# Optimization experiments

Hardware: AMD Instinct MI355X
Metric: run time of the kernel (lower is better)

The kernel has to match this reference:

```python
import jax, jax.numpy as jnp
import numpy as np

B, C, H, W = 16, 512, 64, 64
HEADS = 8
DIL = 2  # dilation of the 3x3 depthwise conv (padding == dilation -> shape preserving)


def setup_inputs() -> dict:
    key = jax.random.key(0)
    ks = jax.random.split(key, 4)
    x = jax.random.normal(ks[0], (B, C, H, W), jnp.float32)
    # kaiming-normal-ish scales (fan_out, relu)
    w_qkv = jax.random.normal(ks[1], (3 * C, C), jnp.float32) * (2.0 / C) ** 0.5  # 1x1 conv weight
    w_dw = jax.random.normal(ks[2], (C, 3, 3), jnp.float32) * (2.0 / 9.0) ** 0.5  # depthwise 3x3
    w_out = jax.random.normal(ks[3], (C, C), jnp.float32) * (2.0 / C) ** 0.5      # 1x1 conv weight
    temperature = jnp.sqrt(jnp.asarray(C // HEADS, jnp.float32))                  # init sqrt(dim_per_head)
    return {"x": x, "w_qkv": w_qkv, "w_dw": w_dw, "w_out": w_out, "temperature": temperature}


def _dw_conv(y, w_dw):
    # depthwise dilated 3x3 conv, padding=dilation -> same spatial size
    rhs = w_dw[:, None, :, :]  # [C,1,3,3]
    return jax.lax.conv_general_dilated(
        y, rhs, window_strides=(1, 1), padding=((DIL, DIL), (DIL, DIL)),
        rhs_dilation=(DIL, DIL), feature_group_count=y.shape[1],
        dimension_numbers=("NCHW", "OIHW", "NCHW"))


def reference(x, w_qkv, w_dw, w_out, temperature):
    b, c, h, w = x.shape
    n = h * w
    d = c // HEADS
    # 1x1 qkv projection (bias-free conv == einsum)
    qkv = jnp.einsum("oc,bchw->bohw", w_qkv, x)  # [B,3C,H,W]
    q, k, v = jnp.split(qkv, 3, axis=1)
    # same depthwise conv applied to q,k,v: fold into batch, conv once
    qkv3 = _dw_conv(jnp.concatenate([q, k, v], axis=0), w_dw)  # [3B,C,H,W]
    q, k, v = jnp.split(qkv3, 3, axis=0)
    q = q.reshape(b, HEADS, d, n)
    k = k.reshape(b, HEADS, d, n)
    v = v.reshape(b, HEADS, d, n)
    # L2 normalize along the per-head channel dim (dim=2), eps=1e-12 like F.normalize
    l2 = lambda t: t / jnp.maximum(jnp.linalg.norm(t, axis=2, keepdims=True), 1e-12)
    q = l2(q)
    k = l2(k)
    # cross-covariance attention: [B,heads,d,d]
    attn = jnp.einsum("bhdn,bhen->bhde", q, k) / jnp.maximum(temperature, 1e-5)
    attn = jax.nn.softmax(attn, axis=-1)
    # dropout is identity in eval mode
    out = jnp.einsum("bhde,bhen->bhdn", attn, v).reshape(b, c, h, w)
    return jnp.einsum("oc,bchw->bohw", w_out, out)
```

## Files before the change

### kernel.cpp

```cpp
#include <hip/hip_runtime.h>

typedef __attribute__((ext_vector_type(8))) short bf16x8;
typedef __attribute__((ext_vector_type(8))) unsigned short ushort8;
typedef __attribute__((ext_vector_type(4))) float f32x4;
typedef __attribute__((ext_vector_type(4))) unsigned int u32x4;
typedef __attribute__((ext_vector_type(2))) unsigned int u32x2;

__device__ __forceinline__ float bf2f(unsigned short u) {
  union { unsigned int i; float f; } v; v.i = ((unsigned int)u) << 16; return v.f;
}
__device__ __forceinline__ float asf(unsigned int u) {
  union { unsigned int i; float f; } v; v.i = u; return v.f;
}
__device__ __forceinline__ unsigned short f2bf(float f) {
  union { float f; unsigned int i; } v; v.f = f;
  unsigned int u = v.i;
  return (unsigned short)((u + 0x7FFFu + ((u >> 16) & 1u)) >> 16);
}
__device__ __forceinline__ void gload16(const void* g, void* l) {
  __builtin_amdgcn_global_load_lds(
      (const __attribute__((address_space(1))) void*)g,
      (__attribute__((address_space(3))) void*)l, 16, 0, 0);
}

__global__ __launch_bounds__(256) void cvt_f32_bf16(const float* __restrict__ s,
                                                    unsigned short* __restrict__ d, int n) {
  int i = blockIdx.x * 256 + threadIdx.x;
  if (i < n) d[i] = f2bf(s[i]);
}

__global__ __launch_bounds__(256) void transpose_x(const float* __restrict__ x,
                                                   unsigned short* __restrict__ xt) {
  __shared__ float tile[64][65];
  const int b = blockIdx.z, ct = blockIdx.y, nt = blockIdx.x;
  const int t = threadIdx.x;
  const int r0 = t >> 6, col = t & 63;
  const float* src = x + ((size_t)b * 512 + ct * 64) * 4096 + nt * 64;
#pragma unroll
  for (int i = 0; i < 16; ++i) {
    int r = i * 4 + r0;
    tile[r][col] = src[(size_t)r * 4096 + col];
  }
  __syncthreads();
  unsigned short* dst = xt + ((size_t)b * 4096 + nt * 64) * 512 + ct * 64;
#pragma unroll
  for (int i = 0; i < 16; ++i) {
    int n = i * 4 + r0;
    dst[(size_t)n * 512 + col] = f2bf(tile[col][n]);
  }
}

__global__ __launch_bounds__(512, 1) void gemm_qkv_8ph(const unsigned short* __restrict__ A,
                                                       const unsigned short* __restrict__ B,
                                                       unsigned short* __restrict__ C) {
  __shared__ unsigned short lA[2][256 * 64];
  __shared__ unsigned short lB[2][256 * 64];
  const int gx = gridDim.x;
  const int nwg = gx * gridDim.y;
  int flat = blockIdx.x + gx * blockIdx.y;
  flat = (flat & 7) * (nwg >> 3) + (flat >> 3);
  const int bx = flat % gx;
  const int by = flat / gx;
  const size_t m0 = (size_t)by * 256;
  const size_t n0 = (size_t)bx * 256;

  const int t = threadIdx.x;
  const int lane = t & 63;
  const int wid = t >> 6;
  const int wm = wid >> 2, wn = wid & 3;
  const int ro = lane & 15, kq = lane >> 4;

  const int srow = t >> 3;
  const int sslot = t & 7;
  const int kslot = sslot ^ (srow & 7);

  auto stageA = [&](int kt, int h, int bbuf) {
    char* d = (char*)(&lA[bbuf][0]) + ((h * 128 + srow) * 64 + sslot * 8) * 2;
    const unsigned short* g = A + (m0 + h * 128 + srow) * 512 + kt * 64 + kslot * 8;
    gload16(g, d);
    gload16(g + (size_t)64 * 512, d + 64 * 128);
  };
  auto stageB = [&](int kt, int h, int bbuf) {
    char* d = (char*)(&lB[bbuf][0]) + ((h * 128 + srow) * 64 + sslot * 8) * 2;
    const unsigned short* g = B + (n0 + h * 128 + srow) * 512 + kt * 64 + kslot * 8;
    gload16(g, d);
    gload16(g + (size_t)64 * 512, d + 64 * 128);
  };

  f32x4 acc[8][4] = {};

  stageA(0, 0, 0); stageA(0, 1, 0);
  stageB(0, 0, 0); stageB(0, 1, 0);
  stageA(1, 0, 1); stageA(1, 1, 1);
  asm volatile("s_waitcnt vmcnt(4)" ::: "memory");
  __builtin_amdgcn_s_barrier();

#pragma unroll 1
  for (int kt = 0; kt < 8; ++kt) {
    const int c = kt & 1;
    const unsigned short* pa = &lA[c][0];
    const unsigned short* pb = &lB[c][0];
    const int slot0 = kq ^ (ro & 7);
    const int slot1 = (4 + kq) ^ (ro & 7);

    bf16x8 a0[8], a1[8], b0, b1, b2, b3;
#pragma unroll
    for (int i = 0; i < 8; ++i)
      a0[i] = *(const bf16x8*)&pa[(wm * 128 + i * 16 + ro) * 64 + slot0 * 8];
    b0 = *(const bf16x8*)&pb[(wn * 64 + 0 * 16 + ro) * 64 + slot0 * 8];
    b1 = *(const bf16x8*)&pb[(wn * 64 + 1 * 16 + ro) * 64 + slot0 * 8];
    if (kt + 1 < 8) stageB(kt + 1, 0, c ^ 1);
    asm volatile("" ::: "memory");
    __builtin_amdgcn_s_barrier();
    asm volatile("s_waitcnt lgkmcnt(0)" ::: "memory");
    __builtin_amdgcn_s_setprio(1);
#pragma unroll
    for (int i = 0; i < 8; ++i) {
      acc[i][0] = __builtin_amdgcn_mfma_f32_16x16x32_bf16(a0[i], b0, acc[i][0], 0, 0, 0);
      acc[i][1] = __builtin_amdgcn_mfma_f32_16x16x32_bf16(a0[i], b1, acc[i][1], 0, 0, 0);
    }
    __builtin_amdgcn_s_setprio(0);

    b2 = *(const bf16x8*)&pb[(wn * 64 + 2 * 16 + ro) * 64 + slot0 * 8];
    b3 = *(const bf16x8*)&pb[(wn * 64 + 3 * 16 + ro) * 64 + slot0 * 8];
    if (kt + 1 < 8) stageB(kt + 1, 1, c ^ 1);
    asm volatile("" ::: "memory");
    __builtin_amdgcn_s_barrier();
    asm volatile("s_waitcnt lgkmcnt(0)" ::: "memory");
    __builtin_amdgcn_s_setprio(1);
#pragma unroll
    for (int i = 0; i < 8; ++i) {
      acc[i][2] = __builtin_amdgcn_mfma_f32_16x16x32_bf16(a0[i], b2, acc[i][2], 0, 0, 0);
      acc[i][3] = __builtin_amdgcn_mfma_f32_16x16x32_bf16(a0[i], b3, acc[i][3], 0, 0, 0);
    }
    __builtin_amdgcn_s_setprio(0);

#pragma unroll
    for (int i = 0; i < 8; ++i)
      a1[i] = *(const bf16x8*)&pa[(wm * 128 + i * 16 + ro) * 64 + slot1 * 8];
    b0 = *(const bf16x8*)&pb[(wn * 64 + 0 * 16 + ro) * 64 + slot1 * 8];
    b1 = *(const bf16x8*)&pb[(wn * 64 + 1 * 16 + ro) * 64 + slot1 * 8];
    asm volatile("s_waitcnt lgkmcnt(0)" ::: "memory");
    __builtin_amdgcn_s_barrier();
    __builtin_amdgcn_s_setprio(1);
#pragma unroll
    for (int i = 0; i < 8; ++i) {
      acc[i][0] = __builtin_amdgcn_mfma_f32_16x16x32_bf16(a1[i], b0, acc[i][0], 0, 0, 0);
      acc[i][1] = __builtin_amdgcn_mfma_f32_16x16x32_bf16(a1[i], b1, acc[i][1], 0, 0, 0);
    }
    __builtin_amdgcn_s_setprio(0);

    b2 = *(const bf16x8*)&pb[(wn * 64 + 2 * 16 + ro) * 64 + slot1 * 8];
    b3 = *(const bf16x8*)&pb[(wn * 64 + 3 * 16 + ro) * 64 + slot1 * 8];
    if (kt + 2 < 8) { stageA(kt + 2, 0, c); stageA(kt + 2, 1, c); }
    asm volatile("s_waitcnt lgkmcnt(0)" ::: "memory");
    if (kt < 6)       asm volatile("s_waitcnt vmcnt(4)" ::: "memory");
    else if (kt == 6) asm volatile("s_waitcnt vmcnt(0)" ::: "memory");
    __builtin_amdgcn_s_barrier();
    __builtin_amdgcn_s_setprio(1);
#pragma unroll
    for (int i = 0; i < 8; ++i) {
      acc[i][2] = __builtin_amdgcn_mfma_f32_16x16x32_bf16(a1[i], b2, acc[i][2], 0, 0, 0);
      acc[i][3] = __builtin_amdgcn_mfma_f32_16x16x32_bf16(a1[i], b3, acc[i][3], 0, 0, 0);
    }
    __builtin_amdgcn_s_setprio(0);
  }

#pragma unroll
  for (int i = 0; i < 8; ++i)
#pragma unroll
    for (int j = 0; j < 4; ++j)
#pragma unroll
      for (int r = 0; r < 4; ++r) {
        size_t row = m0 + wm * 128 + i * 16 + (kq << 2) + r;
        size_t col = n0 + wn * 64 + j * 16 + ro;
        C[row * 1536 + col] = f2bf(acc[i][j][r]);
      }
}

template <bool BF16OUT>
__global__ __launch_bounds__(256) void gemm_bt(const unsigned short* __restrict__ A,
                                               const unsigned short* __restrict__ B,
                                               void* __restrict__ Cv, int K, int ldc,
                                               size_t sA, size_t sB, size_t sC) {
  __shared__ unsigned short lA[2][128 * 32];
  __shared__ unsigned short lB[2][128 * 32];
  const int gx = gridDim.x, gy = gridDim.y;
  const int nwg = gx * gy * gridDim.z;
  int flat = blockIdx.x + gx * (blockIdx.y + gy * blockIdx.z);
  flat = (flat & 7) * (nwg >> 3) + (flat >> 3);
  const int bx = flat % gx;
  const int rem = flat / gx;
  const int by = rem % gy;
  const int bz = rem / gy;

  const int t = threadIdx.x;
  const int lane = t & 63;
  const int wv = t >> 6, wr = wv >> 1, wc = wv & 1;
  const size_t m0 = (size_t)by * 128;
  const size_t n0 = (size_t)bx * 128;
  A += (size_t)bz * sA;
  B += (size_t)bz * sB;
  const unsigned short* ga = A + (m0 + (t >> 2)) * (size_t)K + (t & 3) * 8;
  const unsigned short* gb = B + (n0 + (t >> 2)) * (size_t)K + (t & 3) * 8;
  const size_t gstep = (size_t)64 * K;

  f32x4 acc[4][4] = {};

  auto stage = [&](int kt, int bbuf) {
    const unsigned short* pa = ga + kt * 32;
    const unsigned short* pb = gb + kt * 32;
    char* da = (char*)(&lA[bbuf][0]) + t * 16;
    char* db = (char*)(&lB[bbuf][0]) + t * 16;
    gload16(pa, da);
    gload16(pa + gstep, da + 4096);
    gload16(pb, db);
    gload16(pb + gstep, db + 4096);
  };

  const int nk = K >> 5;
  stage(0, 0);
  __syncthreads();
  int buf = 0;
  for (int kt = 0; kt < nk; ++kt) {
    if (kt + 1 < nk) stage(kt + 1, buf ^ 1);
    const unsigned short* pa = &lA[buf][0];
    const unsigned short* pb = &lB[buf][0];
    const int ro = lane & 15, ko = (lane >> 4) * 8;
    bf16x8 af[4], bv[4];
#pragma unroll
    for (int i = 0; i < 4; ++i) af[i] = *(const bf16x8*)&pa[(wr * 64 + i * 16 + ro) * 32 + ko];
#pragma unroll
    for (int i = 0; i < 4; ++i) bv[i] = *(const bf16x8*)&pb[(wc * 64 + i * 16 + ro) * 32 + ko];
#pragma unroll
    for (int i = 0; i < 4; ++i)
#pragma unroll
      for (int j = 0; j < 4; ++j)
        acc[i][j] = __builtin_amdgcn_mfma_f32_16x16x32_bf16(af[i], bv[j], acc[i][j], 0, 0, 0);
    __syncthreads();
    buf ^= 1;
  }

  if constexpr (BF16OUT) {
    unsigned short* C = (unsigned short*)Cv + (size_t)bz * sC;
#pragma unroll
    for (int i = 0; i < 4; ++i)
#pragma unroll
      for (int j = 0; j < 4; ++j)
#pragma unroll
        for (int r = 0; r < 4; ++r) {
          size_t row = m0 + wr * 64 + i * 16 + ((lane >> 4) << 2) + r;
          size_t col = n0 + wc * 64 + j * 16 + (lane & 15);
          C[row * (size_t)ldc + col] = f2bf(acc[i][j][r]);
        }
  } else {
    float* C = (float*)Cv + (size_t)bz * sC;
#pragma unroll
    for (int i = 0; i < 4; ++i)
#pragma unroll
      for (int j = 0; j < 4; ++j)
#pragma unroll
        for (int r = 0; r < 4; ++r) {
          size_t row = m0 + wr * 64 + i * 16 + ((lane >> 4) << 2) + r;
          size_t col = n0 + wc * 64 + j * 16 + (lane & 15);
          C[row * (size_t)ldc + col] = acc[i][j][r];
        }
  }
}

struct Row3h { u32x2 v[3]; };

__global__ __launch_bounds__(256) void dwconv_norm(const unsigned short* __restrict__ Y,
                                                   const float* __restrict__ wdw,
                                                   unsigned short* __restrict__ Qb,
                                                   unsigned short* __restrict__ Kb,
                                                   unsigned short* __restrict__ Vb) {
  const int t = threadIdx.x, lane = t & 63, wv = t >> 6;
  const int bid = blockIdx.x;
  const int lbid = (bid & 7) * 384 + (bid >> 3);
  const int wid = lbid * 4 + wv;
  const int sub = wid & 3;
  const int x = (wid >> 2) & 63;
  const int grp = wid >> 8;
  const int par = sub >> 1, chhalf = sub & 1;
  const int b = grp / 3, part = grp - b * 3;
  const int c0 = chhalf * 256 + (lane >> 4) * 64 + (lane & 15) * 4;

  float wr[36];
  const float* wp = wdw + c0 * 9;
#pragma unroll
  for (int i = 0; i < 9; ++i) {
    f32x4 q = *(const f32x4*)(wp + i * 4);
    wr[i * 4 + 0] = q[0]; wr[i * 4 + 1] = q[1];
    wr[i * 4 + 2] = q[2]; wr[i * 4 + 3] = q[3];
  }

  const size_t ybase = (size_t)b * 4096 * 1536 + part * 512 + c0;
  const bool okm = (x >= 2), okp = (x <= 61);
  const int xm = okm ? x - 2 : x;
  const int xp = okp ? x + 2 : x;

  auto loadrow = [&](int yy) -> Row3h {
    Row3h r;
    const bool oky = ((unsigned)yy < 64u);
    const int yyc = oky ? yy : 0;
    const size_t rb = ybase + (size_t)(yyc * 64) * 1536;
    u32x2 a = *(const u32x2*)(Y + rb + (size_t)xm * 1536);
    u32x2 c = *(const u32x2*)(Y + rb + (size_t)x * 1536);
    u32x2 d = *(const u32x2*)(Y + rb + (size_t)xp * 1536);
    r.v[0] = a & ((oky && okm) ? 0xFFFFFFFFu : 0u);
    r.v[1] = c & (oky ? 0xFFFFFFFFu : 0u);
    r.v[2] = d & ((oky && okp) ? 0xFFFFFFFFu : 0u);
    return r;
  };

  Row3h W[3];
#pragma unroll
  for (int xt = 0; xt < 3; ++xt) W[0].v[xt] = (u32x2)(0u);
  W[1] = loadrow(par);
  W[2] = loadrow(par + 2);

  unsigned short* dst0 = (part == 0 ? Qb : (part == 1 ? Kb : Vb)) +
                         ((size_t)b * 4096 + x) * 512 + c0;

#pragma unroll
  for (int i = 0; i < 32; ++i) {
    const int y = par + 2 * i;
    float acc[4] = {0.f, 0.f, 0.f, 0.f};
#pragma unroll
    for (int r = 0; r < 3; ++r) {
      const Row3h& R = W[(i + r) % 3];
#pragma unroll
      for (int xt = 0; xt < 3; ++xt) {
        const int tap = r * 3 + xt;
        const u32x2 v = R.v[xt];
#pragma unroll
        for (int m = 0; m < 2; ++m) {
          const unsigned int w2 = v[m];
          acc[2 * m]     += asf(w2 << 16)         * wr[(2 * m) * 9 + tap];
          acc[2 * m + 1] += asf(w2 & 0xFFFF0000u) * wr[(2 * m + 1) * 9 + tap];
        }
      }
    }
    if (part < 2) {
      float ss = 0.f;
#pragma unroll
      for (int j = 0; j < 4; ++j) ss += acc[j] * acc[j];
      ss += __shfl_xor(ss, 1);
      ss += __shfl_xor(ss, 2);
      ss += __shfl_xor(ss, 4);
      ss += __shfl_xor(ss, 8);
      const float rcp = 1.f / fmaxf(sqrtf(ss), 1e-12f);
#pragma unroll
      for (int j = 0; j < 4; ++j) acc[j] *= rcp;
    }
    u32x2 pk;
    pk[0] = (unsigned int)f2bf(acc[0]) | ((unsigned int)f2bf(acc[1]) << 16);
    pk[1] = (unsigned int)f2bf(acc[2]) | ((unsigned int)f2bf(acc[3]) << 16);
    *(u32x2*)(dst0 + (size_t)y * 64 * 512) = pk;
    if (i < 31) W[i % 3] = loadrow(y + 4);
  }
}

__global__ __launch_bounds__(256) void attn_partial(const unsigned short* __restrict__ Qb,
                                                    const unsigned short* __restrict__ Kb,
                                                    float* __restrict__ Spart) {
  __shared__ unsigned short sQ[4][64][72];
  __shared__ unsigned short sK[4][64][72];
  const int t = threadIdx.x, lane = t & 63, wv = t >> 6;
  const int bh = blockIdx.x >> 2;
  const int s = (blockIdx.x & 3) * 4 + wv;
  const int b = bh >> 3, h = bh & 7;
  const unsigned short* qbase = Qb + ((size_t)b * 4096) * 512 + h * 64;
  const unsigned short* kbase = Kb + ((size_t)b * 4096) * 512 + h * 64;
  f32x4 acc[4][4] = {};
  for (int ch = 0; ch < 4; ++ch) {
    const int n0 = s * 256 + ch * 64;
    const unsigned short* qp = qbase + (size_t)(n0 + lane) * 512;
    const unsigned short* kp = kbase + (size_t)(n0 + lane) * 512;
    ushort8 qv[8], kv[8];
#pragma unroll
    for (int v = 0; v < 8; ++v) qv[v] = *(const ushort8*)(qp + v * 8);
#pragma unroll
    for (int v = 0; v < 8; ++v) kv[v] = *(const ushort8*)(kp + v * 8);
#pragma unroll
    for (int v = 0; v < 8; ++v)
#pragma unroll
      for (int j = 0; j < 8; ++j) {
        sQ[wv][v * 8 + j][lane] = qv[v][j];
        sK[wv][v * 8 + j][lane] = kv[v][j];
      }
    __syncthreads();
    const int ro = lane & 15, ko = (lane >> 4) * 8;
#pragma unroll
    for (int ks = 0; ks < 2; ++ks) {
      bf16x8 af[4], bv[4];
#pragma unroll
      for (int i = 0; i < 4; ++i) af[i] = *(const bf16x8*)&sQ[wv][i * 16 + ro][ks * 32 + ko];
#pragma unroll
      for (int i = 0; i < 4; ++i) bv[i] = *(const bf16x8*)&sK[wv][i * 16 + ro][ks * 32 + ko];
#pragma unroll
      for (int i = 0; i < 4; ++i)
#pragma unroll
        for (int j = 0; j < 4; ++j)
          acc[i][j] = __builtin_amdgcn_mfma_f32_16x16x32_bf16(af[i], bv[j], acc[i][j], 0, 0, 0);
    }
    __syncthreads();
  }
  float* dst = Spart + ((size_t)bh * 16 + s) * 4096;
#pragma unroll
  for (int i = 0; i < 4; ++i)
#pragma unroll
    for (int j = 0; j < 4; ++j)
#pragma unroll
      for (int r = 0; r < 4; ++r) {
        int d = i * 16 + ((lane >> 4) << 2) + r;
        int e = j * 16 + (lane & 15);
        dst[d * 64 + e] = acc[i][j][r];
      }
}

__global__ __launch_bounds__(256) void softmax_attn(const float* __restrict__ Spart,
                                                    const float* __restrict__ tptr,
                                                    unsigned short* __restrict__ attn) {
  const int bh = blockIdx.x, t = threadIdx.x;
  const int d = t >> 2, eb = (t & 3) << 4;
  const float inv_t = 1.f / fmaxf(tptr[0], 1e-5f);
  float v[16];
#pragma unroll
  for (int i = 0; i < 16; ++i) v[i] = 0.f;
  for (int s = 0; s < 16; ++s) {
    const f32x4* p = (const f32x4*)(Spart + ((size_t)bh * 16 + s) * 4096 + d * 64 + eb);
#pragma unroll
    for (int i = 0; i < 4; ++i) {
      f32x4 q = p[i];
      v[i * 4 + 0] += q[0]; v[i * 4 + 1] += q[1];
      v[i * 4 + 2] += q[2]; v[i * 4 + 3] += q[3];
    }
  }
  float mx = -1e30f;
#pragma unroll
  for (int i = 0; i < 16; ++i) { v[i] *= inv_t; mx = fmaxf(mx, v[i]); }
  mx = fmaxf(mx, __shfl_xor(mx, 1));
  mx = fmaxf(mx, __shfl_xor(mx, 2));
  float sm = 0.f;
#pragma unroll
  for (int i = 0; i < 16; ++i) { v[i] = __expf(v[i] - mx); sm += v[i]; }
  sm += __shfl_xor(sm, 1);
  sm += __shfl_xor(sm, 2);
  const float r = 1.f / sm;
  ushort8 pk0, pk1;
#pragma unroll
  for (int i = 0; i < 8; ++i) { pk0[i] = f2bf(v[i] * r); pk1[i] = f2bf(v[8 + i] * r); }
  ushort8* dst = (ushort8*)(attn + (size_t)bh * 4096 + d * 64 + eb);
  dst[0] = pk0; dst[1] = pk1;
}

__global__ __launch_bounds__(256) void make_w2(const unsigned short* __restrict__ attn,
                                               const float* __restrict__ w_out,
                                               unsigned short* __restrict__ w2) {
  __shared__ float sA[4096];
  const int bx = blockIdx.x;
  const int bh = bx >> 1, half = bx & 1;
  const int b = bh >> 3, h = bh & 7;
  const int t = threadIdx.x;
  for (int i = t; i < 4096; i += 256) sA[i] = bf2f(attn[(size_t)bh * 4096 + i]);
  __syncthreads();
  const int o = half * 256 + t;
  float w[64];
  const float* wp = w_out + (size_t)o * 512 + h * 64;
#pragma unroll
  for (int i = 0; i < 64; i += 4) {
    f32x4 q = *(const f32x4*)(wp + i);
    w[i] = q[0]; w[i + 1] = q[1]; w[i + 2] = q[2]; w[i + 3] = q[3];
  }
  unsigned short* dst = w2 + ((size_t)b * 512 + o) * 512 + h * 64;
#pragma unroll 1
  for (int eg = 0; eg < 8; ++eg) {
    ushort8 pk;
#pragma unroll
    for (int ee = 0; ee < 8; ++ee) {
      const int e = eg * 8 + ee;
      float acc = 0.f;
#pragma unroll
      for (int dd = 0; dd < 64; ++dd) acc += w[dd] * sA[dd * 64 + e];
      pk[ee] = f2bf(acc);
    }
    *(ushort8*)(dst + eg * 8) = pk;
  }
}

extern "C" void kernel_launch(void* const* d_in, const int* in_sizes, int n_in,
                              void* d_out, int out_size, void* d_ws, size_t ws_size,
                              hipStream_t stream) {
  const float* x     = (const float*)d_in[0];
  const float* w_qkv = (const float*)d_in[1];
  const float* w_dw  = (const float*)d_in[2];
  const float* w_out = (const float*)d_in[3];
  const float* temp  = (const float*)d_in[4];
  float* out = (float*)d_out;

  char* ws = (char*)d_ws;
  const size_t MB = 1024 * 1024;
  unsigned short* Xt    = (unsigned short*)(ws);
  float*          Spart = (float*)(ws);
  unsigned short* attn  = (unsigned short*)(ws + 32 * MB);
  unsigned short* w2    = (unsigned short*)(ws + 33 * MB);
  unsigned short* Y     = (unsigned short*)(ws + 64 * MB);
  unsigned short* Qb    = (unsigned short*)(ws + 256 * MB);
  unsigned short* Kb    = (unsigned short*)(ws + 320 * MB);
  unsigned short* Vb    = (unsigned short*)(ws + 384 * MB);
  unsigned short* Wq    = (unsigned short*)(ws + 448 * MB);

  cvt_f32_bf16<<<3072, 256, 0, stream>>>(w_qkv, Wq, 1536 * 512);
  transpose_x<<<dim3(64, 8, 16), 256, 0, stream>>>(x, Xt);
  gemm_qkv_8ph<<<dim3(6, 256), 512, 0, stream>>>(Xt, Wq, Y);
  dwconv_norm<<<3072, 256, 0, stream>>>(Y, w_dw, Qb, Kb, Vb);
  attn_partial<<<512, 256, 0, stream>>>(Qb, Kb, Spart);
  softmax_attn<<<128, 256, 0, stream>>>(Spart, temp, attn);
  make_w2<<<256, 256, 0, stream>>>(attn, w_out, w2);
  gemm_bt<false><<<dim3(32, 4, 16), 256, 0, stream>>>(
      w2, Vb, out, 512, 4096,
      (size_t)512 * 512, (size_t)4096 * 512, (size_t)512 * 4096);
}
```

Measured before the change: 423.0 us.

## Fuse x transpose and bf16 conversion into QKV GEMM A-tile loading

Removes the separate transpose_x kernel. The QKV GEMM now reads fp32 x directly from its NCHW layout, converts it to bf16 with packed convert instructions and writes it into swizzled LDS through registers, replacing the async global-to-LDS copies. This saves one full write and re-read of the transposed activation tensor plus a kernel launch, at the cost of extra VGPRs, a register-staged A pipeline and reworked vmcnt waits. The depthwise conv kernel is also changed to use packed f32x2 arithmetic and hardware bf16 pack conversion.

```diff
diff --git a/kernel.cpp b/kernel.cpp
--- a/kernel.cpp
+++ b/kernel.cpp
@@ -3,6 +3,7 @@
 typedef __attribute__((ext_vector_type(8))) short bf16x8;
 typedef __attribute__((ext_vector_type(8))) unsigned short ushort8;
 typedef __attribute__((ext_vector_type(4))) float f32x4;
+typedef __attribute__((ext_vector_type(2))) float f32x2;
 typedef __attribute__((ext_vector_type(4))) unsigned int u32x4;
 typedef __attribute__((ext_vector_type(2))) unsigned int u32x2;
 
@@ -29,28 +30,7 @@
   if (i < n) d[i] = f2bf(s[i]);
 }
 
-__global__ __launch_bounds__(256) void transpose_x(const float* __restrict__ x,
-                                                   unsigned short* __restrict__ xt) {
-  __shared__ float tile[64][65];
-  const int b = blockIdx.z, ct = blockIdx.y, nt = blockIdx.x;
-  const int t = threadIdx.x;
-  const int r0 = t >> 6, col = t & 63;
-  const float* src = x + ((size_t)b * 512 + ct * 64) * 4096 + nt * 64;
-#pragma unroll
-  for (int i = 0; i < 16; ++i) {
-    int r = i * 4 + r0;
-    tile[r][col] = src[(size_t)r * 4096 + col];
-  }
-  __syncthreads();
-  unsigned short* dst = xt + ((size_t)b * 4096 + nt * 64) * 512 + ct * 64;
-#pragma unroll
-  for (int i = 0; i < 16; ++i) {
-    int n = i * 4 + r0;
-    dst[(size_t)n * 512 + col] = f2bf(tile[col][n]);
-  }
-}
-
-__global__ __launch_bounds__(512, 1) void gemm_qkv_8ph(const unsigned short* __restrict__ A,
+__global__ __launch_bounds__(512, 1) void gemm_qkv_8ph(const float* __restrict__ X,
                                                        const unsigned short* __restrict__ B,
                                                        unsigned short* __restrict__ C) {
   __shared__ unsigned short lA[2][256 * 64];
@@ -70,16 +50,11 @@
   const int wm = wid >> 2, wn = wid & 3;
   const int ro = lane & 15, kq = lane >> 4;
 
+  const float* xA = X + ((size_t)(m0 >> 12) << 21) + (m0 & 4095);
+
   const int srow = t >> 3;
   const int sslot = t & 7;
   const int kslot = sslot ^ (srow & 7);
-
-  auto stageA = [&](int kt, int h, int bbuf) {
-    char* d = (char*)(&lA[bbuf][0]) + ((h * 128 + srow) * 64 + sslot * 8) * 2;
-    const unsigned short* g = A + (m0 + h * 128 + srow) * 512 + kt * 64 + kslot * 8;
-    gload16(g, d);
-    gload16(g + (size_t)64 * 512, d + 64 * 128);
-  };
   auto stageB = [&](int kt, int h, int bbuf) {
     char* d = (char*)(&lB[bbuf][0]) + ((h * 128 + srow) * 64 + sslot * 8) * 2;
     const unsigned short* g = B + (n0 + h * 128 + srow) * 512 + kt * 64 + kslot * 8;
@@ -87,12 +62,42 @@
     gload16(g + (size_t)64 * 512, d + 64 * 128);
   };
 
+  float av[16];
+  auto loadAh = [&](int kt2, int h) {
+#pragma unroll
+    for (int g2 = 0; g2 < 2; ++g2) {
+      const float* p = xA + (size_t)(kt2 * 64 + wid * 8) * 4096 + h * 128 + g2 * 64 + lane;
+#pragma unroll
+      for (int j = 0; j < 8; ++j)
+        av[g2 * 8 + j] = p[(size_t)j * 4096];
+    }
+  };
+  auto writeAh = [&](int h, int bbuf) {
+#pragma unroll
+    for (int g2 = 0; g2 < 2; ++g2) {
+      unsigned int p0, p1, p2, p3;
+      asm("v_cvt_pk_bf16_f32 %0, %1, %2" : "=v"(p0) : "v"(av[g2*8+0]), "v"(av[g2*8+1]));
+      asm("v_cvt_pk_bf16_f32 %0, %1, %2" : "=v"(p1) : "v"(av[g2*8+2]), "v"(av[g2*8+3]));
+      asm("v_cvt_pk_bf16_f32 %0, %1, %2" : "=v"(p2) : "v"(av[g2*8+4]), "v"(av[g2*8+5]));
+      asm("v_cvt_pk_bf16_f32 %0, %1, %2" : "=v"(p3) : "v"(av[g2*8+6]), "v"(av[g2*8+7]));
+      const int row = h * 128 + g2 * 64 + lane;
+      char* d = (char*)(&lA[bbuf][0]) + row * 128 + (wid ^ (lane & 7)) * 16;
+      u32x4 w4; w4[0] = p0; w4[1] = p1; w4[2] = p2; w4[3] = p3;
+      *(u32x4*)d = w4;
+    }
+  };
+
   f32x4 acc[8][4] = {};
 
-  stageA(0, 0, 0); stageA(0, 1, 0);
   stageB(0, 0, 0); stageB(0, 1, 0);
-  stageA(1, 0, 1); stageA(1, 1, 1);
-  asm volatile("s_waitcnt vmcnt(4)" ::: "memory");
+  loadAh(0, 0);
+  asm volatile("s_waitcnt vmcnt(0)" ::: "memory");
+  writeAh(0, 0);
+  loadAh(0, 1);
+  asm volatile("s_waitcnt vmcnt(0)" ::: "memory");
+  writeAh(1, 0);
+  loadAh(1, 0);
+  asm volatile("s_waitcnt lgkmcnt(0)" ::: "memory");
   __builtin_amdgcn_s_barrier();
 
 #pragma unroll 1
@@ -103,24 +108,30 @@
     const int slot0 = kq ^ (ro & 7);
     const int slot1 = (4 + kq) ^ (ro & 7);
 
-    bf16x8 a0[8], a1[8], b0, b1, b2, b3;
+    bf16x8 a[8], b0, b1;
 #pragma unroll
     for (int i = 0; i < 8; ++i)
-      a0[i] = *(const bf16x8*)&pa[(wm * 128 + i * 16 + ro) * 64 + slot0 * 8];
+      a[i] = *(const bf16x8*)&pa[(wm * 128 + i * 16 + ro) * 64 + slot0 * 8];
     b0 = *(const bf16x8*)&pb[(wn * 64 + 0 * 16 + ro) * 64 + slot0 * 8];
     b1 = *(const bf16x8*)&pb[(wn * 64 + 1 * 16 + ro) * 64 + slot0 * 8];
     if (kt + 1 < 8) stageB(kt + 1, 0, c ^ 1);
     asm volatile("" ::: "memory");
     __builtin_amdgcn_s_barrier();
+    if (kt + 1 < 8) {
+      asm volatile("s_waitcnt vmcnt(0)" ::: "memory");
+      writeAh(0, c ^ 1);
+      loadAh(kt + 1, 1);
+    }
     asm volatile("s_waitcnt lgkmcnt(0)" ::: "memory");
     __builtin_amdgcn_s_setprio(1);
 #pragma unroll
     for (int i = 0; i < 8; ++i) {
-      acc[i][0] = __builtin_amdgcn_mfma_f32_16x16x32_bf16(a0[i], b0, acc[i][0], 0, 0, 0);
-      acc[i][1] = __builtin_amdgcn_mfma_f32_16x16x32_bf16(a0[i], b1, acc[i][1], 0, 0, 0);
+      acc[i][0] = __builtin_amdgcn_mfma_f32_16x16x32_bf16(a[i], b0, acc[i][0], 0, 0, 0);
+      acc[i][1] = __builtin_amdgcn_mfma_f32_16x16x32_bf16(a[i], b1, acc[i][1], 0, 0, 0);
     }
     __builtin_amdgcn_s_setprio(0);
 
+    bf16x8 b2, b3;
     b2 = *(const bf16x8*)&pb[(wn * 64 + 2 * 16 + ro) * 64 + slot0 * 8];
     b3 = *(const bf16x8*)&pb[(wn * 64 + 3 * 16 + ro) * 64 + slot0 * 8];
     if (kt + 1 < 8) stageB(kt + 1, 1, c ^ 1);
@@ -130,38 +141,42 @@
     __builtin_amdgcn_s_setprio(1);
 #pragma unroll
     for (int i = 0; i < 8; ++i) {
-      acc[i][2] = __builtin_amdgcn_mfma_f32_16x16x32_bf16(a0[i], b2, acc[i][2], 0, 0, 0);
-      acc[i][3] = __builtin_amdgcn_mfma_f32_16x16x32_bf16(a0[i], b3, acc[i][3], 0, 0, 0);
+      acc[i][2] = __builtin_amdgcn_mfma_f32_16x16x32_bf16(a[i], b2, acc[i][2], 0, 0, 0);
+      acc[i][3] = __builtin_amdgcn_mfma_f32_16x16x32_bf16(a[i], b3, acc[i][3], 0, 0, 0);
     }
     __builtin_amdgcn_s_setprio(0);
 
 #pragma unroll
     for (int i = 0; i < 8; ++i)
-      a1[i] = *(const bf16x8*)&pa[(wm * 128 + i * 16 + ro) * 64 + slot1 * 8];
+      a[i] = *(const bf16x8*)&pa[(wm * 128 + i * 16 + ro) * 64 + slot1 * 8];
     b0 = *(const bf16x8*)&pb[(wn * 64 + 0 * 16 + ro) * 64 + slot1 * 8];
     b1 = *(const bf16x8*)&pb[(wn * 64 + 1 * 16 + ro) * 64 + slot1 * 8];
     asm volatile("s_waitcnt lgkmcnt(0)" ::: "memory");
     __builtin_amdgcn_s_barrier();
+    if (kt + 1 < 8) {
+      asm volatile("s_waitcnt vmcnt(4)" ::: "memory");
+      writeAh(1, c ^ 1);
+    }
+    if (kt + 2 < 8) loadAh(kt + 2, 0);
     __builtin_amdgcn_s_setprio(1);
 #pragma unroll
     for (int i = 0; i < 8; ++i) {
-      acc[i][0] = __builtin_amdgcn_mfma_f32_16x16x32_bf16(a1[i], b0, acc[i][0], 0, 0, 0);
-      acc[i][1] = __builtin_amdgcn_mfma_f32_16x16x32_bf16(a1[i], b1, acc[i][1], 0, 0, 0);
+      acc[i][0] = __builtin_amdgcn_mfma_f32_16x16x32_bf16(a[i], b0, acc[i][0], 0, 0, 0);
+      acc[i][1] = __builtin_amdgcn_mfma_f32_16x16x32_bf16(a[i], b1, acc[i][1], 0, 0, 0);
     }
     __builtin_amdgcn_s_setprio(0);
 
     b2 = *(const bf16x8*)&pb[(wn * 64 + 2 * 16 + ro) * 64 + slot1 * 8];
     b3 = *(const bf16x8*)&pb[(wn * 64 + 3 * 16 + ro) * 64 + slot1 * 8];
-    if (kt + 2 < 8) { stageA(kt + 2, 0, c); stageA(kt + 2, 1, c); }
     asm volatile("s_waitcnt lgkmcnt(0)" ::: "memory");
-    if (kt < 6)       asm volatile("s_waitcnt vmcnt(4)" ::: "memory");
-    else if (kt == 6) asm volatile("s_waitcnt vmcnt(0)" ::: "memory");
+    if (kt + 2 < 8)      asm volatile("s_waitcnt vmcnt(16)" ::: "memory");
+    else if (kt + 1 < 8) asm volatile("s_waitcnt vmcnt(0)" ::: "memory");
     __builtin_amdgcn_s_barrier();
     __builtin_amdgcn_s_setprio(1);
 #pragma unroll
     for (int i = 0; i < 8; ++i) {
-      acc[i][2] = __builtin_amdgcn_mfma_f32_16x16x32_bf16(a1[i], b2, acc[i][2], 0, 0, 0);
-      acc[i][3] = __builtin_amdgcn_mfma_f32_16x16x32_bf16(a1[i], b3, acc[i][3], 0, 0, 0);
+      acc[i][2] = __builtin_amdgcn_mfma_f32_16x16x32_bf16(a[i], b2, acc[i][2], 0, 0, 0);
+      acc[i][3] = __builtin_amdgcn_mfma_f32_16x16x32_bf16(a[i], b3, acc[i][3], 0, 0, 0);
     }
     __builtin_amdgcn_s_setprio(0);
   }
@@ -286,13 +301,21 @@
   const int b = grp / 3, part = grp - b * 3;
   const int c0 = chhalf * 256 + (lane >> 4) * 64 + (lane & 15) * 4;
 
-  float wr[36];
-  const float* wp = wdw + c0 * 9;
-#pragma unroll
-  for (int i = 0; i < 9; ++i) {
-    f32x4 q = *(const f32x4*)(wp + i * 4);
-    wr[i * 4 + 0] = q[0]; wr[i * 4 + 1] = q[1];
-    wr[i * 4 + 2] = q[2]; wr[i * 4 + 3] = q[3];
+  f32x2 wa[9], wb[9];
+  {
+    float qw[36];
+    const float* wp = wdw + c0 * 9;
+#pragma unroll
+    for (int i = 0; i < 9; ++i) {
+      f32x4 q = *(const f32x4*)(wp + i * 4);
+      qw[i * 4 + 0] = q[0]; qw[i * 4 + 1] = q[1];
+      qw[i * 4 + 2] = q[2]; qw[i * 4 + 3] = q[3];
+    }
+#pragma unroll
+    for (int tap = 0; tap < 9; ++tap) {
+      wa[tap] = (f32x2){qw[tap], qw[9 + tap]};
+      wb[tap] = (f32x2){qw[18 + tap], qw[27 + tap]};
+    }
   }
 
   const size_t ybase = (size_t)b * 4096 * 1536 + part * 512 + c0;
@@ -326,7 +349,7 @@
 #pragma unroll
   for (int i = 0; i < 32; ++i) {
     const int y = par + 2 * i;
-    float acc[4] = {0.f, 0.f, 0.f, 0.f};
+    f32x2 a01 = (f32x2){0.f, 0.f}, a23 = (f32x2){0.f, 0.f};
 #pragma unroll
     for (int r = 0; r < 3; ++r) {
       const Row3h& R = W[(i + r) % 3];
@@ -334,29 +357,26 @@
       for (int xt = 0; xt < 3; ++xt) {
         const int tap = r * 3 + xt;
         const u32x2 v = R.v[xt];
-#pragma unroll
-        for (int m = 0; m < 2; ++m) {
-          const unsigned int w2 = v[m];
-          acc[2 * m]     += asf(w2 << 16)         * wr[(2 * m) * 9 + tap];
-          acc[2 * m + 1] += asf(w2 & 0xFFFF0000u) * wr[(2 * m + 1) * 9 + tap];
-        }
+        f32x2 lo = (f32x2){asf(v[0] << 16), asf(v[0] & 0xFFFF0000u)};
+        f32x2 hi = (f32x2){asf(v[1] << 16), asf(v[1] & 0xFFFF0000u)};
+        a01 += lo * wa[tap];
+        a23 += hi * wb[tap];
       }
     }
     if (part < 2) {
-      float ss = 0.f;
-#pragma unroll
-      for (int j = 0; j < 4; ++j) ss += acc[j] * acc[j];
+      f32x2 s2 = a01 * a01 + a23 * a23;
+      float ss = s2[0] + s2[1];
       ss += __shfl_xor(ss, 1);
       ss += __shfl_xor(ss, 2);
       ss += __shfl_xor(ss, 4);
       ss += __shfl_xor(ss, 8);
       const float rcp = 1.f / fmaxf(sqrtf(ss), 1e-12f);
-#pragma unroll
-      for (int j = 0; j < 4; ++j) acc[j] *= rcp;
-    }
-    u32x2 pk;
-    pk[0] = (unsigned int)f2bf(acc[0]) | ((unsigned int)f2bf(acc[1]) << 16);
-    pk[1] = (unsigned int)f2bf(acc[2]) | ((unsigned int)f2bf(acc[3]) << 16);
+      a01 *= rcp; a23 *= rcp;
+    }
+    unsigned int p0, p1;
+    asm("v_cvt_pk_bf16_f32 %0, %1, %2" : "=v"(p0) : "v"(a01[0]), "v"(a01[1]));
+    asm("v_cvt_pk_bf16_f32 %0, %1, %2" : "=v"(p1) : "v"(a23[0]), "v"(a23[1]));
+    u32x2 pk; pk[0] = p0; pk[1] = p1;
     *(u32x2*)(dst0 + (size_t)y * 64 * 512) = pk;
     if (i < 31) W[i % 3] = loadrow(y + 4);
   }
@@ -502,7 +522,6 @@
 
   char* ws = (char*)d_ws;
   const size_t MB = 1024 * 1024;
-  unsigned short* Xt    = (unsigned short*)(ws);
   float*          Spart = (float*)(ws);
   unsigned short* attn  = (unsigned short*)(ws + 32 * MB);
   unsigned short* w2    = (unsigned short*)(ws + 33 * MB);
@@ -513,8 +532,7 @@
   unsigned short* Wq    = (unsigned short*)(ws + 448 * MB);
 
   cvt_f32_bf16<<<3072, 256, 0, stream>>>(w_qkv, Wq, 1536 * 512);
-  transpose_x<<<dim3(64, 8, 16), 256, 0, stream>>>(x, Xt);
-  gemm_qkv_8ph<<<dim3(6, 256), 512, 0, stream>>>(Xt, Wq, Y);
+  gemm_qkv_8ph<<<dim3(6, 256), 512, 0, stream>>>(x, Wq, Y);
   dwconv_norm<<<3072, 256, 0, stream>>>(Y, w_dw, Qb, Kb, Vb);
   attn_partial<<<512, 256, 0, stream>>>(Qb, Kb, Spart);
   softmax_attn<<<128, 256, 0, stream>>>(Spart, temp, attn);
```

Result: slower. 436.4 us (+3.2%).

## Pack dwconv math into f32x2 ops, use hardware bf16 pack, deepen row prefetch

Applied to the files above, without the earlier changes.

In the transpose kernel, each thread now converts two channels with the hardware v_cvt_pk_bf16_f32 instruction and writes 32-bit pairs instead of single 16-bit stores. In the depthwise conv+norm kernel, the weights are rearranged into f32x2 pairs so the multiply-accumulates can map to packed FMA. The manual bf16 rounding is replaced with the hardware pack instruction. The row ring buffer also grows from 3 to 4 so loads run one extra iteration ahead. The aim is fewer VALU instructions and better hiding of load latency, at the cost of more registers.

```diff
diff --git a/kernel.cpp b/kernel.cpp
--- a/kernel.cpp
+++ b/kernel.cpp
@@ -3,6 +3,7 @@
 typedef __attribute__((ext_vector_type(8))) short bf16x8;
 typedef __attribute__((ext_vector_type(8))) unsigned short ushort8;
 typedef __attribute__((ext_vector_type(4))) float f32x4;
+typedef __attribute__((ext_vector_type(2))) float f32x2;
 typedef __attribute__((ext_vector_type(4))) unsigned int u32x4;
 typedef __attribute__((ext_vector_type(2))) unsigned int u32x2;
 
@@ -43,10 +44,14 @@
   }
   __syncthreads();
   unsigned short* dst = xt + ((size_t)b * 4096 + nt * 64) * 512 + ct * 64;
-#pragma unroll
-  for (int i = 0; i < 16; ++i) {
-    int n = i * 4 + r0;
-    dst[(size_t)n * 512 + col] = f2bf(tile[col][n]);
+  const int c2 = (t & 31) * 2;
+  const int nsub = t >> 5;
+#pragma unroll
+  for (int i = 0; i < 8; ++i) {
+    int n = i * 8 + nsub;
+    unsigned int p;
+    asm("v_cvt_pk_bf16_f32 %0, %1, %2" : "=v"(p) : "v"(tile[c2][n]), "v"(tile[c2 + 1][n]));
+    *(unsigned int*)(dst + (size_t)n * 512 + c2) = p;
   }
 }
 
@@ -286,13 +291,21 @@
   const int b = grp / 3, part = grp - b * 3;
   const int c0 = chhalf * 256 + (lane >> 4) * 64 + (lane & 15) * 4;
 
-  float wr[36];
-  const float* wp = wdw + c0 * 9;
-#pragma unroll
-  for (int i = 0; i < 9; ++i) {
-    f32x4 q = *(const f32x4*)(wp + i * 4);
-    wr[i * 4 + 0] = q[0]; wr[i * 4 + 1] = q[1];
-    wr[i * 4 + 2] = q[2]; wr[i * 4 + 3] = q[3];
+  f32x2 wa[9], wb[9];
+  {
+    float qw[36];
+    const float* wp = wdw + c0 * 9;
+#pragma unroll
+    for (int i = 0; i < 9; ++i) {
+      f32x4 q = *(const f32x4*)(wp + i * 4);
+      qw[i * 4 + 0] = q[0]; qw[i * 4 + 1] = q[1];
+      qw[i * 4 + 2] = q[2]; qw[i * 4 + 3] = q[3];
+    }
+#pragma unroll
+    for (int tap = 0; tap < 9; ++tap) {
+      wa[tap] = (f32x2){qw[tap], qw[9 + tap]};
+      wb[tap] = (f32x2){qw[18 + tap], qw[27 + tap]};
+    }
   }
 
   const size_t ybase = (size_t)b * 4096 * 1536 + part * 512 + c0;
@@ -314,11 +327,12 @@
     return r;
   };
 
-  Row3h W[3];
+  Row3h W[4];
 #pragma unroll
   for (int xt = 0; xt < 3; ++xt) W[0].v[xt] = (u32x2)(0u);
   W[1] = loadrow(par);
   W[2] = loadrow(par + 2);
+  W[3] = loadrow(par + 4);
 
   unsigned short* dst0 = (part == 0 ? Qb : (part == 1 ? Kb : Vb)) +
                          ((size_t)b * 4096 + x) * 512 + c0;
@@ -326,39 +340,36 @@
 #pragma unroll
   for (int i = 0; i < 32; ++i) {
     const int y = par + 2 * i;
-    float acc[4] = {0.f, 0.f, 0.f, 0.f};
+    f32x2 a01 = (f32x2){0.f, 0.f}, a23 = (f32x2){0.f, 0.f};
 #pragma unroll
     for (int r = 0; r < 3; ++r) {
-      const Row3h& R = W[(i + r) % 3];
+      const Row3h& R = W[(i + r) & 3];
 #pragma unroll
       for (int xt = 0; xt < 3; ++xt) {
         const int tap = r * 3 + xt;
         const u32x2 v = R.v[xt];
-#pragma unroll
-        for (int m = 0; m < 2; ++m) {
-          const unsigned int w2 = v[m];
-          acc[2 * m]     += asf(w2 << 16)         * wr[(2 * m) * 9 + tap];
-          acc[2 * m + 1] += asf(w2 & 0xFFFF0000u) * wr[(2 * m + 1) * 9 + tap];
-        }
+        f32x2 lo = (f32x2){asf(v[0] << 16), asf(v[0] & 0xFFFF0000u)};
+        f32x2 hi = (f32x2){asf(v[1] << 16), asf(v[1] & 0xFFFF0000u)};
+        a01 += lo * wa[tap];
+        a23 += hi * wb[tap];
       }
     }
     if (part < 2) {
-      float ss = 0.f;
-#pragma unroll
-      for (int j = 0; j < 4; ++j) ss += acc[j] * acc[j];
+      f32x2 s2 = a01 * a01 + a23 * a23;
+      float ss = s2[0] + s2[1];
       ss += __shfl_xor(ss, 1);
       ss += __shfl_xor(ss, 2);
       ss += __shfl_xor(ss, 4);
       ss += __shfl_xor(ss, 8);
       const float rcp = 1.f / fmaxf(sqrtf(ss), 1e-12f);
-#pragma unroll
-      for (int j = 0; j < 4; ++j) acc[j] *= rcp;
-    }
-    u32x2 pk;
-    pk[0] = (unsigned int)f2bf(acc[0]) | ((unsigned int)f2bf(acc[1]) << 16);
-    pk[1] = (unsigned int)f2bf(acc[2]) | ((unsigned int)f2bf(acc[3]) << 16);
+      a01 *= rcp; a23 *= rcp;
+    }
+    unsigned int p0, p1;
+    asm("v_cvt_pk_bf16_f32 %0, %1, %2" : "=v"(p0) : "v"(a01[0]), "v"(a01[1]));
+    asm("v_cvt_pk_bf16_f32 %0, %1, %2" : "=v"(p1) : "v"(a23[0]), "v"(a23[1]));
+    u32x2 pk; pk[0] = p0; pk[1] = p1;
     *(u32x2*)(dst0 + (size_t)y * 64 * 512) = pk;
-    if (i < 31) W[i % 3] = loadrow(y + 4);
+    if (i < 30) W[i & 3] = loadrow(y + 6);
   }
 }
 
```

New measurement: 413.0 us. 1.02x faster.
